# Kernel optimization log

Hardware: AMD Instinct MI355X
Metric: run time of the kernel (lower is better)

The kernel has to match this reference:

```python
import jax, jax.numpy as jnp
import numpy as np

B, L, D, H, R = 4, 4096, 1024, 16, 30
DK = D // H  # 64
EPS = 1e-12  # torch F.normalize eps


def setup_inputs() -> dict:
    key = jax.random.key(0)
    ks = jax.random.split(key, 16)
    n = lambda k, shp, s=0.02: jax.random.normal(k, shp, jnp.float32) * s
    return {
        "queries": jax.random.normal(ks[0], (B, L, D), jnp.float32),
        "keys": jax.random.normal(ks[1], (B, L, D), jnp.float32),
        "values": jax.random.normal(ks[2], (B, L, D), jnp.float32),
        # linear weights stored as (in, out); equivalent to torch y = x @ W.T + b
        "Wq": n(ks[3], (D, D)), "bq": jnp.zeros((D,), jnp.float32),
        "Wk": n(ks[4], (D, D)), "bk": jnp.zeros((D,), jnp.float32),
        "We": n(ks[5], (H, DK, R), 0.1),
        "Wr": n(ks[6], (H, DK, R), 0.1),
        "Lam": jax.random.uniform(ks[7], (H, R), jnp.float32),
        "Wc": n(ks[8], (2 * R, DK)), "bc": jnp.zeros((DK,), jnp.float32),
        "Wo": n(ks[9], (D, D)), "bo": jnp.zeros((D,), jnp.float32),
    }


def _l2norm(x):
    nrm = jnp.sqrt(jnp.sum(x * x, axis=-1, keepdims=True))
    return x / jnp.maximum(nrm, EPS)


def reference(queries, keys, values, Wq, bq, Wk, bk, We, Wr, Lam, Wc, bc, Wo, bo):
    b, l, _ = queries.shape
    # projections -> [B, H, L, DK]
    q = (queries @ Wq + bq).reshape(b, l, H, DK).transpose(0, 2, 1, 3)
    k = (keys @ Wk + bk).reshape(b, l, H, DK).transpose(0, 2, 1, 3)
    # causal cumulative mean over sequence
    normal = (jnp.arange(l, dtype=jnp.float32) + 1.0)[None, None, :, None]
    q = jnp.cumsum(q, axis=2) / normal
    k = jnp.cumsum(k, axis=2) / normal
    # L2-normalized feature map
    q = _l2norm(q)
    k = _l2norm(k)
    # per-head low-rank projections -> [B, H, L, R]
    escore = jnp.einsum('bhld,hdr->bhlr', q, We)
    rscore = jnp.einsum('bhld,hdr->bhlr', k, Wr)
    score = jnp.concatenate([escore, rscore], axis=-1)  # [B, H, L, 2R]
    out = score @ Wc + bc                                # [B, H, L, DK]
    out = out.transpose(0, 2, 1, 3).reshape(b, l, H * DK)
    out = out @ Wo + bo                                  # [B, L, D]
    # dropout is identity in eval mode
    return (out, escore, rscore, Lam)
```

## Files before the change

### kernel.cpp

```cpp
#include <hip/hip_runtime.h>
#include <hip/hip_bf16.h>

#define BATCH 4
#define LSEQ 4096
#define DMODEL 1024
#define NHEAD 16
#define RDIM 30
#define DKH 64
#define NCHUNK 32
#define CHUNK 128

typedef __attribute__((ext_vector_type(8))) short bf16x8_t;
typedef __attribute__((ext_vector_type(4))) float f32x4_t;

static __device__ __forceinline__ unsigned short f2bf(float f) {
    __hip_bfloat16 h = __float2bfloat16(f);
    unsigned short u;
    __builtin_memcpy(&u, &h, 2);
    return u;
}
static __device__ __forceinline__ float b2f(unsigned short u) {
    unsigned v = ((unsigned)u) << 16;
    float f;
    __builtin_memcpy(&f, &v, 4);
    return f;
}

#define SWAIT_VM8()   { asm volatile("s_waitcnt vmcnt(8)" ::: "memory"); __builtin_amdgcn_sched_barrier(0); }
#define SWAIT_VM4()   { asm volatile("s_waitcnt vmcnt(4)" ::: "memory"); __builtin_amdgcn_sched_barrier(0); }
#define SWAIT_VM0()   { asm volatile("s_waitcnt vmcnt(0)" ::: "memory"); __builtin_amdgcn_sched_barrier(0); }
#define SWAIT_LGKM0() { asm volatile("s_waitcnt lgkmcnt(0)" ::: "memory"); __builtin_amdgcn_sched_barrier(0); }
#define SBARRIER()    { __builtin_amdgcn_s_barrier(); __builtin_amdgcn_sched_barrier(0); }

__global__ void transpose_cvt_kernel(const float* __restrict__ W0, const float* __restrict__ W1,
                                     unsigned short* __restrict__ O0, unsigned short* __restrict__ O1) {
    __shared__ float tile[32][33];
    const float* W = blockIdx.z ? W1 : W0;
    unsigned short* outT = blockIdx.z ? O1 : O0;
    int n0 = blockIdx.x * 32, k0 = blockIdx.y * 32;
    int tx = threadIdx.x, ty = threadIdx.y;
    #pragma unroll
    for (int r = ty; r < 32; r += 8)
        tile[r][tx] = W[(size_t)(k0 + r) * DMODEL + n0 + tx];
    __syncthreads();
    #pragma unroll
    for (int r = ty; r < 32; r += 8)
        outT[(size_t)(n0 + r) * DMODEL + k0 + tx] = f2bf(tile[tx][r]);
}

__global__ void wpack_kernel(const float* __restrict__ We, const float* __restrict__ Wr,
                             unsigned short* __restrict__ WeP, unsigned short* __restrict__ WrP) {
    int h = blockIdx.x;
    const float* W = blockIdx.y ? Wr : We;
    unsigned short* O = blockIdx.y ? WrP : WeP;
    for (int idx = threadIdx.x; idx < 2048; idx += 256) {
        int col = idx >> 6, k = idx & 63;
        float v = (col < RDIM) ? W[((size_t)h * 64 + k) * RDIM + col] : 0.f;
        O[((size_t)h << 11) + idx] = f2bf(v);
    }
}

__global__ __launch_bounds__(256) void bias2_kernel(
    const float* __restrict__ Wo, const float* __restrict__ bc,
    const float* __restrict__ bo, float* __restrict__ bias2) {
    __shared__ float red[4][64];
    const int n = blockIdx.x * 64 + (threadIdx.x & 63);
    const int dg = threadIdx.x >> 6;
    float a = 0.f;
    #pragma unroll 4
    for (int d = dg * 256; d < dg * 256 + 256; ++d)
        a = fmaf(bc[d & 63], Wo[(size_t)d * DMODEL + n], a);
    red[dg][threadIdx.x & 63] = a;
    __syncthreads();
    if (dg == 0)
        bias2[n] = bo[n] + red[0][threadIdx.x] + red[1][threadIdx.x]
                         + red[2][threadIdx.x] + red[3][threadIdx.x];
}

__global__ __launch_bounds__(256) void wfold_kernel(
    const float* __restrict__ Wc, const float* __restrict__ Wo,
    unsigned short* __restrict__ WfoldT)
{
    __shared__ float WoT[64][65];
    __shared__ float WcT[64][61];
    const int tid = threadIdx.x;
    const int n0 = blockIdx.x * 64, h = blockIdx.y;
    for (int i = tid; i < 4096; i += 256) {
        int dk = i >> 6, n = i & 63;
        WoT[dk][n] = Wo[(size_t)(h * 64 + dk) * DMODEL + n0 + n];
    }
    for (int i = tid; i < 3840; i += 256) {
        int j = i >> 6, dk = i & 63;
        WcT[dk][j] = Wc[j * 64 + dk];
    }
    __syncthreads();
    #pragma unroll 1
    for (int oo = 0; oo < 16; ++oo) {
        int n = (tid >> 6) + oo * 4;
        int j = tid & 63;
        int jr = (j < 30) ? j : (j >= 32 && j < 62) ? (j - 2) : -1;
        float acc = 0.f;
        if (jr >= 0) {
            #pragma unroll
            for (int dk = 0; dk < 64; ++dk)
                acc = fmaf(WcT[dk][jr], WoT[dk][n], acc);
        }
        WfoldT[(size_t)(n0 + n) * 1024 + h * 64 + j] = f2bf(acc);
    }
}

#define GBM 256
#define GBN 256

template <bool AF32, bool BF16_OUT, bool DOCUM, int KD>
__global__ __launch_bounds__(512, 2) void gemm8_kernel(
    const void* __restrict__ Av0, const void* __restrict__ Av1,
    const unsigned short* __restrict__ Bt0, const unsigned short* __restrict__ Bt1,
    const float* __restrict__ bias0, const float* __restrict__ bias1,
    void* __restrict__ Cv0, void* __restrict__ Cv1,
    float* __restrict__ part0, float* __restrict__ part1,
    int N)
{
    constexpr int NT = KD / 64;
    __shared__ __align__(16) unsigned short As[2][GBM * 64];
    __shared__ __align__(16) unsigned short Bs[2][GBM * 64];
    const int tid = threadIdx.x;
    const int lane = tid & 63;
    const int wid = tid >> 6;
    const int wm = wid >> 2;
    const int wn = wid & 3;
    const int lm = lane & 15;
    const int kb = lane >> 4;
    const int z = blockIdx.z;

    const void* Av = z ? Av1 : Av0;
    const unsigned short* Bt = z ? Bt1 : Bt0;
    const float* bias = z ? bias1 : bias0;
    void* Cv = z ? Cv1 : Cv0;
    float* part = z ? part1 : part0;

    const int nwg = gridDim.x * gridDim.y;
    const int wg = blockIdx.y * gridDim.x + blockIdx.x;
    const int cpx = nwg >> 3;
    const int swz = (wg & 7) * cpx + (wg >> 3);
    const int bn = swz % gridDim.x;
    const int bm = swz / gridDim.x;

    const unsigned short* Btile = Bt + (size_t)(bn * GBN) * KD;
    const float* A32_tile = nullptr;
    const unsigned short* A16_tile = nullptr;
    if constexpr (AF32) A32_tile = (const float*)Av + (size_t)(bm * GBM) * KD;
    else                A16_tile = (const unsigned short*)Av + (size_t)(bm * GBM) * KD;

    f32x4_t acc[8][4];
    #pragma unroll
    for (int i = 0; i < 8; ++i)
        #pragma unroll
        for (int j = 0; j < 4; ++j)
            acc[i][j] = f32x4_t{0.f, 0.f, 0.f, 0.f};

    auto B_STAGE = [&](int buf, int kt) {
        #pragma unroll
        for (int seg = 0; seg < 4; ++seg) {
            const int s = (seg << 13) + (tid << 4);
            const int row = s >> 7;
            const int cc = ((s >> 4) & 7) ^ (row & 7);
            const unsigned short* gb = Btile + (size_t)row * KD + kt * 64 + cc * 8;
            __builtin_amdgcn_global_load_lds(
                (const __attribute__((address_space(1))) void*)gb,
                (__attribute__((address_space(3))) void*)((char*)&Bs[buf][0] + (seg << 13) + (wid << 10)),
                16, 0, 0);
        }
    };
    auto A_STAGE16 = [&](int buf, int kt) {
        #pragma unroll
        for (int seg = 0; seg < 4; ++seg) {
            const int s = (seg << 13) + (tid << 4);
            const int row = s >> 7;
            const int cc = ((s >> 4) & 7) ^ (row & 7);
            const unsigned short* ga = A16_tile + (size_t)row * KD + kt * 64 + cc * 8;
            __builtin_amdgcn_global_load_lds(
                (const __attribute__((address_space(1))) void*)ga,
                (__attribute__((address_space(3))) void*)((char*)&As[buf][0] + (seg << 13) + (wid << 10)),
                16, 0, 0);
        }
    };
    float4 areg[8];
    auto A_ISSUE = [&](int kt) {
        #pragma unroll
        for (int p = 0; p < 8; ++p) {
            int q = p * 512 + tid;
            int row = q >> 4, kq = q & 15;
            areg[p] = *(const float4*)(A32_tile + (size_t)row * KD + kt * 64 + kq * 4);
        }
    };
    auto A_WRITE = [&](int buf) {
        #pragma unroll
        for (int p = 0; p < 8; ++p) {
            int q = p * 512 + tid;
            int row = q >> 4, kq = q & 15;
            ushort4 pk;
            pk.x = f2bf(areg[p].x); pk.y = f2bf(areg[p].y);
            pk.z = f2bf(areg[p].z); pk.w = f2bf(areg[p].w);
            int cc = (kq >> 1) ^ (row & 7);
            *(ushort4*)((char*)&As[buf][0] + row * 128 + (cc << 4) + (kq & 1) * 8) = pk;
        }
    };

    bf16x8_t af[8], bfr[4];
    auto LOADFRAGS = [&](int buf, int ks) {
        #pragma unroll
        for (int i = 0; i < 8; ++i) {
            int row = wm * 128 + i * 16 + lm;
            int cc = (ks * 4 + kb) ^ (row & 7);
            af[i] = *(const bf16x8_t*)((const char*)&As[buf][0] + row * 128 + cc * 16);
        }
        #pragma unroll
        for (int j = 0; j < 4; ++j) {
            int row = wn * 64 + j * 16 + lm;
            int cc = (ks * 4 + kb) ^ (row & 7);
            bfr[j] = *(const bf16x8_t*)((const char*)&Bs[buf][0] + row * 128 + cc * 16);
        }
    };
    auto MFMAC = [&]() {
        __builtin_amdgcn_s_setprio(1);
        #pragma unroll
        for (int i = 0; i < 8; ++i)
            #pragma unroll
            for (int j = 0; j < 4; ++j)
                acc[i][j] = __builtin_amdgcn_mfma_f32_16x16x32_bf16(af[i], bfr[j], acc[i][j], 0, 0, 0);
        __builtin_amdgcn_s_setprio(0);
    };

    if constexpr (AF32) {
        B_STAGE(0, 0);
        A_ISSUE(0);
        SWAIT_VM0();
        A_WRITE(0);
        B_STAGE(1, 1);
        A_ISSUE(1);
        SWAIT_LGKM0();
        SBARRIER();
    } else {
        A_STAGE16(0, 0);
        B_STAGE(0, 0);
        __builtin_amdgcn_sched_barrier(0);
        A_STAGE16(1, 1);
        B_STAGE(1, 1);
        SWAIT_VM8();
        SBARRIER();
    }

    int cur = 0;
    for (int t = 0; t < NT; ++t) {
        LOADFRAGS(cur, 0);
        MFMAC();
        LOADFRAGS(cur, 1);
        SWAIT_LGKM0();
        SBARRIER();
        if constexpr (AF32) {
            if (t + 2 < NT) B_STAGE(cur, t + 2);
            if (t + 1 < NT) {
                if (t + 2 < NT) { SWAIT_VM4(); }
                else            { SWAIT_VM0(); }
                A_WRITE(cur ^ 1);
                if (t + 2 < NT) A_ISSUE(t + 2);
            }
            MFMAC();
            if (t + 1 < NT) { SWAIT_LGKM0(); SBARRIER(); }
        } else {
            if (t + 2 < NT) { A_STAGE16(cur, t + 2); B_STAGE(cur, t + 2); }
            MFMAC();
            if (t + 1 < NT) {
                if (t + 2 < NT) { SWAIT_VM8(); }
                else            { SWAIT_VM0(); }
                SBARRIER();
            }
        }
        cur ^= 1;
    }

    if constexpr (DOCUM) {
        const int g = lane >> 4;
        const int row0 = bm * GBM + wm * 128;
        #pragma unroll
        for (int j = 0; j < 4; ++j) {
            const int col = bn * GBN + wn * 64 + j * 16 + lm;
            const float bv = bias[col];
            float tot[8], x16[8], x32s[8];
            #pragma unroll
            for (int i = 0; i < 8; ++i) {
                float c0 = acc[i][j][0] + bv;
                float c1 = c0 + acc[i][j][1] + bv;
                float c2 = c1 + acc[i][j][2] + bv;
                float c3 = c2 + acc[i][j][3] + bv;
                acc[i][j][0] = c0; acc[i][j][1] = c1; acc[i][j][2] = c2; acc[i][j][3] = c3;
                tot[i] = c3;
            }
            #pragma unroll
            for (int i = 0; i < 8; ++i) x16[i] = __shfl_xor(tot[i], 16);
            #pragma unroll
            for (int i = 0; i < 8; ++i) x32s[i] = __shfl_xor(tot[i] + x16[i], 32);
            float runbase = 0.f;
            #pragma unroll
            for (int i = 0; i < 8; ++i) {
                float pre = ((g & 1) ? x16[i] : 0.f) + ((g & 2) ? x32s[i] : 0.f);
                float base2 = runbase + pre;
                runbase += tot[i] + x16[i] + x32s[i];
                acc[i][j][0] += base2; acc[i][j][1] += base2;
                acc[i][j][2] += base2; acc[i][j][3] += base2;
            }
            if (g == 0)
                part[((size_t)(row0 >> 7) << 10) + col] = runbase;
        }
        #pragma unroll
        for (int i = 0; i < 8; ++i) {
            int row = row0 + i * 16 + g * 4;
            #pragma unroll
            for (int j = 0; j < 4; ++j) {
                int col = bn * GBN + wn * 64 + j * 16 + lm;
                unsigned short* cp = (unsigned short*)Cv + (size_t)row * N + col;
                cp[0]             = f2bf(acc[i][j][0]);
                cp[(size_t)N]     = f2bf(acc[i][j][1]);
                cp[(size_t)2 * N] = f2bf(acc[i][j][2]);
                cp[(size_t)3 * N] = f2bf(acc[i][j][3]);
            }
        }
    } else {
        #pragma unroll
        for (int i = 0; i < 8; ++i) {
            int row = bm * GBM + wm * 128 + i * 16 + (lane >> 4) * 4;
            #pragma unroll
            for (int j = 0; j < 4; ++j) {
                int col = bn * GBN + wn * 64 + j * 16 + lm;
                float bv = bias[col];
                #pragma unroll
                for (int r = 0; r < 4; ++r) {
                    float v = acc[i][j][r] + bv;
                    if constexpr (BF16_OUT)
                        ((unsigned short*)Cv)[(size_t)(row + r) * N + col] = f2bf(v);
                    else
                        ((float*)Cv)[(size_t)(row + r) * N + col] = v;
                }
            }
        }
    }
}

__global__ __launch_bounds__(256) void chunk_offsets_kernel(float* __restrict__ partQ, float* __restrict__ partK)
{
    int t = blockIdx.x * 256 + threadIdx.x;
    float* part = blockIdx.y ? partK : partQ;
    int b = t >> 10, d = t & 1023;
    size_t base = ((size_t)b * NCHUNK) * DMODEL + d;
    float v[NCHUNK];
    #pragma unroll
    for (int c = 0; c < NCHUNK; ++c)
        v[c] = part[base + (size_t)c * DMODEL];
    float run = 0.f;
    #pragma unroll
    for (int c = 0; c < NCHUNK; ++c) {
        float x = v[c];
        v[c] = run;
        run += x;
    }
    #pragma unroll
    for (int c = 0; c < NCHUNK; ++c)
        part[base + (size_t)c * DMODEL] = v[c];
}

__global__ __launch_bounds__(256) void score_kernel(
    const unsigned short* __restrict__ Qc, const unsigned short* __restrict__ Kc,
    const float* __restrict__ partQ, const float* __restrict__ partK,
    const unsigned short* __restrict__ WeP, const unsigned short* __restrict__ WrP,
    float* __restrict__ escore, float* __restrict__ rscore,
    unsigned short* __restrict__ sbf)
{
    __shared__ float n2buf[4][64];
    const int tid = threadIdx.x;
    const int lane = tid & 63;
    const int w = tid >> 6;
    const int lm = lane & 15;
    const int lk = lane >> 4;
    const int c = blockIdx.x;
    const int bh = blockIdx.y;
    const int z = blockIdx.z;
    const int b = bh >> 4, h = bh & 15;
    const unsigned short* X = z ? Kc : Qc;
    const float* part = z ? partK : partQ;
    const unsigned short* WP = z ? WrP : WeP;
    float* eout = z ? rscore : escore;
    const int row0 = c * 256 + w * 64;
    const int co = c * 2 + (w >> 1);

    const float* offp = part + ((size_t)(b * NCHUNK + co)) * DMODEL + h * 64 + lk * 8;
    float o0[8], o1[8];
    {
        float4 a = *(const float4*)(offp);
        float4 bb = *(const float4*)(offp + 4);
        float4 cc = *(const float4*)(offp + 32);
        float4 dd = *(const float4*)(offp + 36);
        o0[0] = a.x; o0[1] = a.y; o0[2] = a.z; o0[3] = a.w;
        o0[4] = bb.x; o0[5] = bb.y; o0[6] = bb.z; o0[7] = bb.w;
        o1[0] = cc.x; o1[1] = cc.y; o1[2] = cc.z; o1[3] = cc.w;
        o1[4] = dd.x; o1[5] = dd.y; o1[6] = dd.z; o1[7] = dd.w;
    }

    const unsigned short* wpb = WP + ((size_t)h << 11) + lm * 64 + lk * 8;
    bf16x8_t b00 = *(const bf16x8_t*)(wpb);
    bf16x8_t b01 = *(const bf16x8_t*)(wpb + 32);
    bf16x8_t b10 = *(const bf16x8_t*)(wpb + 16 * 64);
    bf16x8_t b11 = *(const bf16x8_t*)(wpb + 16 * 64 + 32);

    f32x4_t acc[4][2];
    float n2p[4];
    #pragma unroll
    for (int i = 0; i < 4; ++i) {
        n2p[i] = 0.f;
        acc[i][0] = f32x4_t{0.f, 0.f, 0.f, 0.f};
        acc[i][1] = f32x4_t{0.f, 0.f, 0.f, 0.f};
    }

    const unsigned short* xbase = X + ((size_t)(b * LSEQ + row0 + lm)) * DMODEL + h * 64 + lk * 8;
    #pragma unroll
    for (int i = 0; i < 4; ++i) {
        const unsigned short* xp = xbase + (size_t)(16 * i) * DMODEL;
        bf16x8_t x0 = *(const bf16x8_t*)(xp);
        bf16x8_t x1 = *(const bf16x8_t*)(xp + 32);
        bf16x8_t xa0, xa1;
        #pragma unroll
        for (int j = 0; j < 8; ++j) {
            float xf = b2f((unsigned short)x0[j]) + o0[j];
            n2p[i] = fmaf(xf, xf, n2p[i]);
            xa0[j] = (short)f2bf(xf);
        }
        #pragma unroll
        for (int j = 0; j < 8; ++j) {
            float xf = b2f((unsigned short)x1[j]) + o1[j];
            n2p[i] = fmaf(xf, xf, n2p[i]);
            xa1[j] = (short)f2bf(xf);
        }
        acc[i][0] = __builtin_amdgcn_mfma_f32_16x16x32_bf16(xa0, b00, acc[i][0], 0, 0, 0);
        acc[i][1] = __builtin_amdgcn_mfma_f32_16x16x32_bf16(xa0, b10, acc[i][1], 0, 0, 0);
        acc[i][0] = __builtin_amdgcn_mfma_f32_16x16x32_bf16(xa1, b01, acc[i][0], 0, 0, 0);
        acc[i][1] = __builtin_amdgcn_mfma_f32_16x16x32_bf16(xa1, b11, acc[i][1], 0, 0, 0);
    }

    #pragma unroll
    for (int i = 0; i < 4; ++i) {
        n2p[i] += __shfl_xor(n2p[i], 16);
        n2p[i] += __shfl_xor(n2p[i], 32);
    }
    if (lane < 16) {
        #pragma unroll
        for (int i = 0; i < 4; ++i) n2buf[w][16 * i + lane] = n2p[i];
    }
    __syncthreads();

    #pragma unroll
    for (int i = 0; i < 4; ++i) {
        f32x4_t n2v = *(const f32x4_t*)&n2buf[w][16 * i + lk * 4];
        float inv[4];
        #pragma unroll
        for (int r = 0; r < 4; ++r) {
            int lr = row0 + 16 * i + lk * 4 + r;
            inv[r] = 1.f / fmaxf(sqrtf(n2v[r]), 1e-12f * (float)(lr + 1));
        }
        #pragma unroll
        for (int j = 0; j < 2; ++j) {
            int col = 16 * j + lm;
            #pragma unroll
            for (int r = 0; r < 4; ++r) {
                int lr = row0 + 16 * i + lk * 4 + r;
                float v = acc[i][j][r] * inv[r];
                if (col < RDIM)
                    eout[(((size_t)(b * NHEAD + h)) * LSEQ + lr) * RDIM + col] = v;
                sbf[((size_t)(b * LSEQ + lr)) * 1024 + h * 64 + z * 32 + col] =
                    (col < RDIM) ? f2bf(v) : (unsigned short)0;
            }
        }
    }
}

extern "C" void kernel_launch(void* const* d_in, const int* in_sizes, int n_in,
                              void* d_out, int out_size, void* d_ws, size_t ws_size,
                              hipStream_t stream)
{
    const float* queries = (const float*)d_in[0];
    const float* keys    = (const float*)d_in[1];
    const float* Wq = (const float*)d_in[3];
    const float* bq = (const float*)d_in[4];
    const float* Wk = (const float*)d_in[5];
    const float* bk = (const float*)d_in[6];
    const float* We = (const float*)d_in[7];
    const float* Wr = (const float*)d_in[8];
    const float* Lam = (const float*)d_in[9];
    const float* Wc = (const float*)d_in[10];
    const float* bc = (const float*)d_in[11];
    const float* Wo = (const float*)d_in[12];
    const float* bo = (const float*)d_in[13];

    float* out = (float*)d_out;
    float* escore = out + (size_t)16777216;
    float* rscore = out + (size_t)24641536;
    float* lam_out = out + (size_t)32505856;

    char* ws = (char*)d_ws;
    unsigned short* sbf = (unsigned short*)ws;
    unsigned short* Qb  = (unsigned short*)(ws + 33554432);
    unsigned short* Kb  = (unsigned short*)(ws + 67108864);
    unsigned short* WqT = (unsigned short*)(ws + 100663296);
    unsigned short* WkT = (unsigned short*)(ws + 102760448);
    unsigned short* WfT = (unsigned short*)(ws + 104857600);
    float* bias2 = (float*)(ws + 106954752);
    float* partQ = (float*)(ws + 106958848);
    float* partK = (float*)(ws + 107483136);
    unsigned short* WeP = (unsigned short*)(ws + 108007424);
    unsigned short* WrP = (unsigned short*)(ws + 108072960);

    dim3 tb(32, 8);
    transpose_cvt_kernel<<<dim3(32, 32, 2), tb, 0, stream>>>(Wq, Wk, WqT, WkT);
    wpack_kernel<<<dim3(16, 2), 256, 0, stream>>>(We, Wr, WeP, WrP);
    bias2_kernel<<<16, 256, 0, stream>>>(Wo, bc, bo, bias2);
    wfold_kernel<<<dim3(16, 16), 256, 0, stream>>>(Wc, Wo, WfT);

    gemm8_kernel<true, true, true, 1024><<<dim3(4, 64, 2), 512, 0, stream>>>(
        queries, keys, WqT, WkT, bq, bk, Qb, Kb, partQ, partK, 1024);

    chunk_offsets_kernel<<<dim3(16, 2), 256, 0, stream>>>(partQ, partK);

    score_kernel<<<dim3(16, 64, 2), 256, 0, stream>>>(Qb, Kb, partQ, partK, WeP, WrP,
                                                      escore, rscore, sbf);

    gemm8_kernel<false, false, false, 1024><<<dim3(4, 64, 1), 512, 0, stream>>>(
        sbf, sbf, WfT, WfT, bias2, bias2, out, out, nullptr, nullptr, 1024);

    hipMemcpyAsync(lam_out, Lam, 480 * sizeof(float), hipMemcpyDeviceToDevice, stream);
}
```

Measured before the change: 267.4 us.

## Merge weight-prep kernels into one launch and double-buffer fp32 A prefetch in GEMM

Four small weight-preparation kernels (transpose/convert, We/Wr packing, bias fold, Wc·Wo fold) are combined into a single prep_kernel launch that dispatches on block index, removing three launch gaps. In the fp32-A GEMM path, A prefetch now uses two register sets that alternate across a two-step unrolled loop. The global load for tile t+2 is therefore issued earlier, before the barrier, and the vmcnt wait is relaxed to 12. This hides more global-load latency at the cost of eight extra float4 registers per thread, which could increase register pressure at 512 threads with two blocks per CU.

```diff
diff --git a/kernel.cpp b/kernel.cpp
--- a/kernel.cpp
+++ b/kernel.cpp
@@ -26,86 +26,88 @@
     return f;
 }
 
+#define SWAIT_VM12()  { asm volatile("s_waitcnt vmcnt(12)" ::: "memory"); __builtin_amdgcn_sched_barrier(0); }
 #define SWAIT_VM8()   { asm volatile("s_waitcnt vmcnt(8)" ::: "memory"); __builtin_amdgcn_sched_barrier(0); }
-#define SWAIT_VM4()   { asm volatile("s_waitcnt vmcnt(4)" ::: "memory"); __builtin_amdgcn_sched_barrier(0); }
 #define SWAIT_VM0()   { asm volatile("s_waitcnt vmcnt(0)" ::: "memory"); __builtin_amdgcn_sched_barrier(0); }
 #define SWAIT_LGKM0() { asm volatile("s_waitcnt lgkmcnt(0)" ::: "memory"); __builtin_amdgcn_sched_barrier(0); }
 #define SBARRIER()    { __builtin_amdgcn_s_barrier(); __builtin_amdgcn_sched_barrier(0); }
 
-__global__ void transpose_cvt_kernel(const float* __restrict__ W0, const float* __restrict__ W1,
-                                     unsigned short* __restrict__ O0, unsigned short* __restrict__ O1) {
-    __shared__ float tile[32][33];
-    const float* W = blockIdx.z ? W1 : W0;
-    unsigned short* outT = blockIdx.z ? O1 : O0;
-    int n0 = blockIdx.x * 32, k0 = blockIdx.y * 32;
-    int tx = threadIdx.x, ty = threadIdx.y;
-    #pragma unroll
-    for (int r = ty; r < 32; r += 8)
-        tile[r][tx] = W[(size_t)(k0 + r) * DMODEL + n0 + tx];
-    __syncthreads();
-    #pragma unroll
-    for (int r = ty; r < 32; r += 8)
-        outT[(size_t)(n0 + r) * DMODEL + k0 + tx] = f2bf(tile[tx][r]);
-}
-
-__global__ void wpack_kernel(const float* __restrict__ We, const float* __restrict__ Wr,
-                             unsigned short* __restrict__ WeP, unsigned short* __restrict__ WrP) {
-    int h = blockIdx.x;
-    const float* W = blockIdx.y ? Wr : We;
-    unsigned short* O = blockIdx.y ? WrP : WeP;
-    for (int idx = threadIdx.x; idx < 2048; idx += 256) {
-        int col = idx >> 6, k = idx & 63;
-        float v = (col < RDIM) ? W[((size_t)h * 64 + k) * RDIM + col] : 0.f;
-        O[((size_t)h << 11) + idx] = f2bf(v);
-    }
-}
-
-__global__ __launch_bounds__(256) void bias2_kernel(
-    const float* __restrict__ Wo, const float* __restrict__ bc,
-    const float* __restrict__ bo, float* __restrict__ bias2) {
-    __shared__ float red[4][64];
-    const int n = blockIdx.x * 64 + (threadIdx.x & 63);
-    const int dg = threadIdx.x >> 6;
-    float a = 0.f;
-    #pragma unroll 4
-    for (int d = dg * 256; d < dg * 256 + 256; ++d)
-        a = fmaf(bc[d & 63], Wo[(size_t)d * DMODEL + n], a);
-    red[dg][threadIdx.x & 63] = a;
-    __syncthreads();
-    if (dg == 0)
-        bias2[n] = bo[n] + red[0][threadIdx.x] + red[1][threadIdx.x]
-                         + red[2][threadIdx.x] + red[3][threadIdx.x];
-}
-
-__global__ __launch_bounds__(256) void wfold_kernel(
+__global__ __launch_bounds__(256) void prep_kernel(
+    const float* __restrict__ Wq, const float* __restrict__ Wk,
+    unsigned short* __restrict__ WqT, unsigned short* __restrict__ WkT,
+    const float* __restrict__ We, const float* __restrict__ Wr,
+    unsigned short* __restrict__ WeP, unsigned short* __restrict__ WrP,
     const float* __restrict__ Wc, const float* __restrict__ Wo,
-    unsigned short* __restrict__ WfoldT)
+    unsigned short* __restrict__ WfoldT,
+    const float* __restrict__ bc, const float* __restrict__ bo,
+    float* __restrict__ bias2)
 {
-    __shared__ float WoT[64][65];
-    __shared__ float WcT[64][61];
+    __shared__ __align__(16) char lmem[32256];
+    const int bid = blockIdx.x;
     const int tid = threadIdx.x;
-    const int n0 = blockIdx.x * 64, h = blockIdx.y;
-    for (int i = tid; i < 4096; i += 256) {
-        int dk = i >> 6, n = i & 63;
-        WoT[dk][n] = Wo[(size_t)(h * 64 + dk) * DMODEL + n0 + n];
-    }
-    for (int i = tid; i < 3840; i += 256) {
-        int j = i >> 6, dk = i & 63;
-        WcT[dk][j] = Wc[j * 64 + dk];
-    }
-    __syncthreads();
-    #pragma unroll 1
-    for (int oo = 0; oo < 16; ++oo) {
-        int n = (tid >> 6) + oo * 4;
-        int j = tid & 63;
-        int jr = (j < 30) ? j : (j >= 32 && j < 62) ? (j - 2) : -1;
-        float acc = 0.f;
-        if (jr >= 0) {
-            #pragma unroll
-            for (int dk = 0; dk < 64; ++dk)
-                acc = fmaf(WcT[dk][jr], WoT[dk][n], acc);
-        }
-        WfoldT[(size_t)(n0 + n) * 1024 + h * 64 + j] = f2bf(acc);
+    if (bid < 2048) {
+        float (*tile)[33] = (float(*)[33])lmem;
+        const float* W = (bid >= 1024) ? Wk : Wq;
+        unsigned short* outT = (bid >= 1024) ? WkT : WqT;
+        int rem = bid & 1023;
+        int n0 = (rem & 31) * 32, k0 = (rem >> 5) * 32;
+        int tx = tid & 31, ty = tid >> 5;
+        #pragma unroll
+        for (int r = ty; r < 32; r += 8)
+            tile[r][tx] = W[(size_t)(k0 + r) * DMODEL + n0 + tx];
+        __syncthreads();
+        #pragma unroll
+        for (int r = ty; r < 32; r += 8)
+            outT[(size_t)(n0 + r) * DMODEL + k0 + tx] = f2bf(tile[tx][r]);
+    } else if (bid < 2080) {
+        int idx0 = bid - 2048;
+        int h = idx0 >> 1;
+        const float* W = (idx0 & 1) ? Wr : We;
+        unsigned short* O = (idx0 & 1) ? WrP : WeP;
+        for (int idx = tid; idx < 2048; idx += 256) {
+            int col = idx >> 6, k = idx & 63;
+            float v = (col < RDIM) ? W[((size_t)h * 64 + k) * RDIM + col] : 0.f;
+            O[((size_t)h << 11) + idx] = f2bf(v);
+        }
+    } else if (bid < 2096) {
+        float (*red)[64] = (float(*)[64])lmem;
+        const int n = (bid - 2080) * 64 + (tid & 63);
+        const int dg = tid >> 6;
+        float a = 0.f;
+        #pragma unroll 4
+        for (int d = dg * 256; d < dg * 256 + 256; ++d)
+            a = fmaf(bc[d & 63], Wo[(size_t)d * DMODEL + n], a);
+        red[dg][tid & 63] = a;
+        __syncthreads();
+        if (dg == 0)
+            bias2[n] = bo[n] + red[0][tid] + red[1][tid] + red[2][tid] + red[3][tid];
+    } else {
+        float (*WoT)[65] = (float(*)[65])lmem;
+        float (*WcT)[61] = (float(*)[61])(lmem + 16640);
+        int idx0 = bid - 2096;
+        const int n0 = (idx0 & 15) * 64, h = idx0 >> 4;
+        for (int i = tid; i < 4096; i += 256) {
+            int dk = i >> 6, n = i & 63;
+            WoT[dk][n] = Wo[(size_t)(h * 64 + dk) * DMODEL + n0 + n];
+        }
+        for (int i = tid; i < 3840; i += 256) {
+            int j = i >> 6, dk = i & 63;
+            WcT[dk][j] = Wc[j * 64 + dk];
+        }
+        __syncthreads();
+        #pragma unroll 1
+        for (int oo = 0; oo < 16; ++oo) {
+            int n = (tid >> 6) + oo * 4;
+            int j = tid & 63;
+            int jr = (j < 30) ? j : (j >= 32 && j < 62) ? (j - 2) : -1;
+            float acc = 0.f;
+            if (jr >= 0) {
+                #pragma unroll
+                for (int dk = 0; dk < 64; ++dk)
+                    acc = fmaf(WcT[dk][jr], WoT[dk][n], acc);
+            }
+            WfoldT[(size_t)(n0 + n) * 1024 + h * 64 + j] = f2bf(acc);
+        }
     }
 }
 
@@ -185,23 +187,22 @@
                 16, 0, 0);
         }
     };
-    float4 areg[8];
-    auto A_ISSUE = [&](int kt) {
+    auto A_ISSUE = [&](int kt, float4 (&ar)[8]) {
         #pragma unroll
         for (int p = 0; p < 8; ++p) {
             int q = p * 512 + tid;
             int row = q >> 4, kq = q & 15;
-            areg[p] = *(const float4*)(A32_tile + (size_t)row * KD + kt * 64 + kq * 4);
+            ar[p] = *(const float4*)(A32_tile + (size_t)row * KD + kt * 64 + kq * 4);
         }
     };
-    auto A_WRITE = [&](int buf) {
+    auto A_WRITE = [&](int buf, float4 (&ar)[8]) {
         #pragma unroll
         for (int p = 0; p < 8; ++p) {
             int q = p * 512 + tid;
             int row = q >> 4, kq = q & 15;
             ushort4 pk;
-            pk.x = f2bf(areg[p].x); pk.y = f2bf(areg[p].y);
-            pk.z = f2bf(areg[p].z); pk.w = f2bf(areg[p].w);
+            pk.x = f2bf(ar[p].x); pk.y = f2bf(ar[p].y);
+            pk.z = f2bf(ar[p].z); pk.w = f2bf(ar[p].w);
             int cc = (kq >> 1) ^ (row & 7);
             *(ushort4*)((char*)&As[buf][0] + row * 128 + (cc << 4) + (kq & 1) * 8) = pk;
         }
@@ -233,14 +234,37 @@
     };
 
     if constexpr (AF32) {
+        float4 aregA[8], aregB[8];
         B_STAGE(0, 0);
-        A_ISSUE(0);
+        A_ISSUE(0, aregB);
         SWAIT_VM0();
-        A_WRITE(0);
+        A_WRITE(0, aregB);
         B_STAGE(1, 1);
-        A_ISSUE(1);
+        A_ISSUE(1, aregA);
         SWAIT_LGKM0();
         SBARRIER();
+
+        auto ITER = [&](int t, int cur, float4 (&P)[8], float4 (&Q)[8]) {
+            LOADFRAGS(cur, 0);
+            MFMAC();
+            LOADFRAGS(cur, 1);
+            if (t + 2 < NT) A_ISSUE(t + 2, Q);
+            SWAIT_LGKM0();
+            SBARRIER();
+            if (t + 2 < NT) B_STAGE(cur, t + 2);
+            if (t + 1 < NT) {
+                if (t + 2 < NT) { SWAIT_VM12(); }
+                else            { SWAIT_VM0(); }
+                A_WRITE(cur ^ 1, P);
+            }
+            MFMAC();
+            if (t + 1 < NT) { SWAIT_LGKM0(); SBARRIER(); }
+        };
+        #pragma unroll 1
+        for (int tt = 0; tt < NT; tt += 2) {
+            ITER(tt,     0, aregA, aregB);
+            ITER(tt + 1, 1, aregB, aregA);
+        }
     } else {
         A_STAGE16(0, 0);
         B_STAGE(0, 0);
@@ -249,26 +273,14 @@
         B_STAGE(1, 1);
         SWAIT_VM8();
         SBARRIER();
-    }
-
-    int cur = 0;
-    for (int t = 0; t < NT; ++t) {
-        LOADFRAGS(cur, 0);
-        MFMAC();
-        LOADFRAGS(cur, 1);
-        SWAIT_LGKM0();
-        SBARRIER();
-        if constexpr (AF32) {
-            if (t + 2 < NT) B_STAGE(cur, t + 2);
-            if (t + 1 < NT) {
-                if (t + 2 < NT) { SWAIT_VM4(); }
-                else            { SWAIT_VM0(); }
-                A_WRITE(cur ^ 1);
-                if (t + 2 < NT) A_ISSUE(t + 2);
-            }
+        int cur = 0;
+        #pragma unroll 1
+        for (int t = 0; t < NT; ++t) {
+            LOADFRAGS(cur, 0);
             MFMAC();
-            if (t + 1 < NT) { SWAIT_LGKM0(); SBARRIER(); }
-        } else {
+            LOADFRAGS(cur, 1);
+            SWAIT_LGKM0();
+            SBARRIER();
             if (t + 2 < NT) { A_STAGE16(cur, t + 2); B_STAGE(cur, t + 2); }
             MFMAC();
             if (t + 1 < NT) {
@@ -276,8 +288,8 @@
                 else            { SWAIT_VM0(); }
                 SBARRIER();
             }
-        }
-        cur ^= 1;
+            cur ^= 1;
+        }
     }
 
     if constexpr (DOCUM) {
@@ -518,11 +530,8 @@
     unsigned short* WeP = (unsigned short*)(ws + 108007424);
     unsigned short* WrP = (unsigned short*)(ws + 108072960);
 
-    dim3 tb(32, 8);
-    transpose_cvt_kernel<<<dim3(32, 32, 2), tb, 0, stream>>>(Wq, Wk, WqT, WkT);
-    wpack_kernel<<<dim3(16, 2), 256, 0, stream>>>(We, Wr, WeP, WrP);
-    bias2_kernel<<<16, 256, 0, stream>>>(Wo, bc, bo, bias2);
-    wfold_kernel<<<dim3(16, 16), 256, 0, stream>>>(Wc, Wo, WfT);
+    prep_kernel<<<2352, 256, 0, stream>>>(Wq, Wk, WqT, WkT, We, Wr, WeP, WrP,
+                                          Wc, Wo, WfT, bc, bo, bias2);
 
     gemm8_kernel<true, true, true, 1024><<<dim3(4, 64, 2), 512, 0, stream>>>(
         queries, keys, WqT, WkT, bq, bk, Qb, Kb, partQ, partK, 1024);
```

After: 628.6 us. +135.1%, slower.
